# Kernel tuning notes

Measured on AMD Instinct MI355X. Metric: run time of the kernel, lower is better.

The kernel has to match this reference:

```python
import jax, jax.numpy as jnp
import numpy as np

IMAGE_SIZE = 128
FACES_PER_PIXEL = 4
BLUR_RADIUS = 0.01
EPS = 1e-8


def setup_inputs() -> dict:
    key = jax.random.key(0)
    k1, k2, k3 = jax.random.split(key, 3)
    B, V, F = 2, 2000, 800
    # verts are already projected to screen/NDC space: x,y in [-1,1], z > 0 (depth)
    xy = jax.random.uniform(k1, (B, V, 2), minval=-1.0, maxval=1.0)
    z = jax.random.uniform(k2, (B, V, 1), minval=0.5, maxval=2.5)
    verts = jnp.concatenate([xy, z], axis=-1).astype(jnp.float32)
    faces = jax.random.randint(k3, (F, 3), 0, V)
    return {"verts": verts, "faces": faces}


def _edge(a, b, p):
    # signed parallelogram area of (a -> b -> p), using xy components only
    return (p[..., 0] - a[..., 0]) * (b[..., 1] - a[..., 1]) - (
        p[..., 1] - a[..., 1]) * (b[..., 0] - a[..., 0])


def _seg_dist2(p, a, b):
    # squared distance from point p to segment [a, b] in 2D
    ab = b - a
    pa = p - a
    t = jnp.clip(jnp.sum(pa * ab, -1) / (jnp.sum(ab * ab, -1) + EPS), 0.0, 1.0)
    d = pa - t[..., None] * ab
    return jnp.sum(d * d, -1)


def _rasterize(verts, faces):
    H = W = IMAGE_SIZE
    K = FACES_PER_PIXEL
    B = verts.shape[0]
    fv = verts[:, faces]                      # [B,F,3,3] gather face vertices
    v0, v1, v2 = fv[:, :, 0], fv[:, :, 1], fv[:, :, 2]
    a0 = v0[:, None, :, :2]                   # [B,1,F,2]
    a1 = v1[:, None, :, :2]
    a2 = v2[:, None, :, :2]
    z0 = v0[:, None, :, 2]                    # [B,1,F]
    z1 = v1[:, None, :, 2]
    z2 = v2[:, None, :, 2]
    # pixel centers in NDC, pytorch3d convention: index 0 -> +1, last -> -1
    xs = 1.0 - 2.0 * (jnp.arange(W, dtype=verts.dtype) + 0.5) / W
    ys = 1.0 - 2.0 * (jnp.arange(H, dtype=verts.dtype) + 0.5) / H
    yy, xx = jnp.meshgrid(ys, xs, indexing="ij")
    p = jnp.stack([xx, yy], -1).reshape(1, -1, 1, 2)   # [1,P,1,2], P=H*W

    area = _edge(a0, a1, a2)                  # [B,1,F] signed face area*2
    w0 = _edge(a1, a2, p)                     # [B,P,F]
    w1 = _edge(a2, a0, p)
    w2 = _edge(a0, a1, p)
    denom = jnp.where(jnp.abs(area) > EPS, area,
                      jnp.where(area >= 0, EPS, -EPS))
    b0, b1, b2 = w0 / denom, w1 / denom, w2 / denom
    zpix = b0 * z0 + b1 * z1 + b2 * z2        # [B,P,F] interpolated depth

    inside = (b0 >= 0) & (b1 >= 0) & (b2 >= 0)
    dmin = jnp.minimum(_seg_dist2(p, a0, a1),
                       jnp.minimum(_seg_dist2(p, a1, a2),
                                   _seg_dist2(p, a2, a0)))
    dsign = jnp.where(inside, -dmin, dmin)    # signed squared edge distance

    valid = (inside | (dmin < BLUR_RADIUS)) & (zpix > EPS) & (
        jnp.abs(area) > EPS)
    zcand = jnp.where(valid, zpix, jnp.inf)
    _, idx = jax.lax.top_k(-zcand, K)         # K nearest faces per pixel

    take = lambda x: jnp.take_along_axis(x, idx, axis=-1)
    sel_valid = take(valid)
    pix_to_face = jnp.where(sel_valid, idx, -1)
    zbuf = jnp.where(sel_valid, take(zpix), -1.0)
    bary = jnp.stack([b0, b1, b2], -1)        # [B,P,F,3]
    bsel = jnp.take_along_axis(bary, idx[..., None], axis=2)  # [B,P,K,3]
    bsel = jnp.where(sel_valid[..., None], bsel, -1.0)
    dsel = jnp.where(sel_valid, take(dsign), -1.0)

    return (pix_to_face.reshape(B, H, W, K),
            zbuf.reshape(B, H, W, K),
            bsel.reshape(B, H, W, K, 3),
            dsel.reshape(B, H, W, K))


def reference(verts, faces):
    # Fragments: (pix_to_face, zbuf, bary_coords, dists)
    return _rasterize(verts, faces)
```

## Files before the change

### kernel.cpp

```cpp
#include <hip/hip_runtime.h>

#define IMG   128
#define KF    4
#define NF    800
#define NV    2000
#define NB    2
#define EPSF  1e-8f
#define BLURF 0.01f
#define CULL_D2 0.0103f
#define HEXT    0.0547f

typedef unsigned long long u64;
#define INVK ((((u64)0x7f800000u) << 32) | 0xffffffffu)

#pragma clang fp contract(off)

__device__ __forceinline__ float seg_d2(float pax, float pay, float abx, float aby) {
#pragma clang fp contract(off)
    float dd = (abx * abx + aby * aby) + EPSF;
    float t  = (pax * abx + pay * aby) / dd;
    t = fminf(fmaxf(t, 0.0f), 1.0f);
    float dx = pax - t * abx;
    float dy = pay - t * aby;
    return dx * dx + dy * dy;
}

__device__ __forceinline__ void ins4(u64& s0, u64& s1, u64& s2, u64& s3, u64 k) {
    bool c0 = k < s0, c1 = k < s1, c2 = k < s2, c3 = k < s3;
    s3 = c2 ? s2 : (c3 ? k : s3);
    s2 = c1 ? s1 : (c2 ? k : s2);
    s1 = c0 ? s0 : (c1 ? k : s1);
    s0 = c0 ? k  : s0;
}

__global__ __launch_bounds__(256) void raster_p1(
    const float* __restrict__ verts,
    const int*   __restrict__ faces,
    u64* __restrict__ ws,
    int sh)
{
#pragma clang fp contract(off)
    extern __shared__ char dynLDS[];
    __shared__ u64 sK[2 * 4 * 64];
    __shared__ int sTot;

    const int S     = 1 << sh;
    const int chunk = NF >> sh;
    float* sFD  = (float*)dynLDS;
    int*   sList = (int*)(dynLDS + (size_t)chunk * 10 * sizeof(float));

    const int tid   = threadIdx.x;
    const int blk   = blockIdx.x;
    const int tile  = blk >> sh;
    const int slice = blk & (S - 1);
    const int b     = tile >> 8;
    const int trow  = (tile & 255) >> 4;
    const int tcol  = tile & 15;
    const float* vb = verts + b * NV * 3;
    const int fbase = slice * chunk;

    if (tid == 0) sTot = 0;

    for (int j = tid; j < chunk; j += 256) {
        int f = fbase + j;
        int i0 = faces[3 * f + 0], i1 = faces[3 * f + 1], i2 = faces[3 * f + 2];
        float a0x = vb[3 * i0], a0y = vb[3 * i0 + 1], z0 = vb[3 * i0 + 2];
        float a1x = vb[3 * i1], a1y = vb[3 * i1 + 1], z1 = vb[3 * i1 + 2];
        float a2x = vb[3 * i2], a2y = vb[3 * i2 + 1], z2 = vb[3 * i2 + 2];
        float area = (a2x - a0x) * (a1y - a0y) - (a2y - a0y) * (a1x - a0x);
        float aab  = fabsf(area);
        float denom = (aab > EPSF) ? area : (area >= 0.0f ? EPSF : -EPSF);
        float* fd = &sFD[j * 10];
        fd[0] = a0x; fd[1] = a0y; fd[2] = a1x; fd[3] = a1y; fd[4] = a2x; fd[5] = a2y;
        fd[6] = z0;  fd[7] = z1;  fd[8] = z2;  fd[9] = denom;
    }
    __syncthreads();

    const int wave = tid >> 6;
    const int lane = tid & 63;
    const int pr = lane >> 3, pc = lane & 7;
    const int row = trow * 8 + pr, col = tcol * 8 + pc;
    const float px = 1.0f - (2.0f * ((float)col + 0.5f)) / 128.0f;
    const float py = 1.0f - (2.0f * ((float)row + 0.5f)) / 128.0f;
    const float txmax = 1.0f - (2.0f * ((float)(tcol * 8)     + 0.5f)) / 128.0f;
    const float txmin = 1.0f - (2.0f * ((float)(tcol * 8 + 7) + 0.5f)) / 128.0f;
    const float tymax = 1.0f - (2.0f * ((float)(trow * 8)     + 0.5f)) / 128.0f;
    const float tymin = 1.0f - (2.0f * ((float)(trow * 8 + 7) + 0.5f)) / 128.0f;
    const float cx = 0.5f * (txmin + txmax);
    const float cy = 0.5f * (tymin + tymax);

    for (int j = tid; j < chunk; j += 256) {
        const float* fd = &sFD[j * 10];
        float a0x = fd[0], a0y = fd[1], a1x = fd[2], a1y = fd[3], a2x = fd[4], a2y = fd[5];
        float area = (a2x - a0x) * (a1y - a0y) - (a2y - a0y) * (a1x - a0x);
        bool surv = fabsf(area) > EPSF;
        float bxmin = fminf(a0x, fminf(a1x, a2x)) - 0.101f;
        float bxmax = fmaxf(a0x, fmaxf(a1x, a2x)) + 0.101f;
        float bymin = fminf(a0y, fminf(a1y, a2y)) - 0.101f;
        float bymax = fmaxf(a0y, fmaxf(a1y, a2y)) + 0.101f;
        surv &= !(bxmin > txmax || bxmax < txmin || bymin > tymax || bymax < tymin);
        float s = (area >= 0.0f) ? 1.0f : -1.0f;
        float e0x = a2x - a1x, e0y = a2y - a1y;
        float e1x = a0x - a2x, e1y = a0y - a2y;
        float e2x = a1x - a0x, e2y = a1y - a0y;
        float w0 = s * ((cx - a1x) * e0y - (cy - a1y) * e0x) + HEXT * (fabsf(e0x) + fabsf(e0y));
        float w1 = s * ((cx - a2x) * e1y - (cy - a2y) * e1x) + HEXT * (fabsf(e1x) + fabsf(e1y));
        float w2 = s * ((cx - a0x) * e2y - (cy - a0y) * e2x) + HEXT * (fabsf(e2x) + fabsf(e2y));
        float l0 = e0x * e0x + e0y * e0y;
        float l1 = e1x * e1x + e1y * e1y;
        float l2 = e2x * e2x + e2y * e2y;
        surv &= !((w0 < 0.0f) & (w0 * w0 > CULL_D2 * l0));
        surv &= !((w1 < 0.0f) & (w1 * w1 > CULL_D2 * l1));
        surv &= !((w2 < 0.0f) & (w2 * w2 > CULL_D2 * l2));
        if (surv) {
            int pos = atomicAdd(&sTot, 1);
            sList[pos] = j;
        }
    }
    __syncthreads();
    const int total = sTot;

    u64 s0 = INVK, s1 = INVK, s2 = INVK, s3 = INVK;
    for (int j = wave; j < total; j += 4) {
        int lf = sList[j];
        const float* fd = &sFD[lf * 10];
        float a0x = fd[0], a0y = fd[1], a1x = fd[2], a1y = fd[3], a2x = fd[4], a2y = fd[5];
        float z0 = fd[6], z1 = fd[7], z2 = fd[8], denom = fd[9];
        float e0x = a2x - a1x, e0y = a2y - a1y;
        float e1x = a0x - a2x, e1y = a0y - a2y;
        float e2x = a1x - a0x, e2y = a1y - a0y;
        float p0x = px - a0x, p0y = py - a0y;
        float p1x = px - a1x, p1y = py - a1y;
        float p2x = px - a2x, p2y = py - a2y;
        float w0 = p1x * e0y - p1y * e0x;
        float w1 = p2x * e1y - p2y * e1x;
        float w2 = p0x * e2y - p0y * e2x;
        float b0 = w0 / denom, b1 = w1 / denom, b2 = w2 / denom;
        float zpix = (b0 * z0 + b1 * z1) + b2 * z2;
        bool inside = fminf(b0, fminf(b1, b2)) >= 0.0f;
        bool valid;
        if (__all(inside)) {
            valid = (zpix > EPSF);
        } else {
            float dA = seg_d2(p0x, p0y, e2x, e2y);
            float dB = seg_d2(p1x, p1y, e0x, e0y);
            float dC = seg_d2(p2x, p2y, e1x, e1y);
            float dmin = fminf(dA, fminf(dB, dC));
            valid = (inside | (dmin < BLURF)) & (zpix > EPSF);
        }
        u64 key = valid ? ((((u64)__float_as_uint(zpix)) << 32) | (unsigned)(fbase + lf)) : INVK;
        if (__any(key < s3)) ins4(s0, s1, s2, s3, key);
    }

    if (wave >= 2) {
        int r = wave - 2;
        sK[(r * 4 + 0) * 64 + lane] = s0;
        sK[(r * 4 + 1) * 64 + lane] = s1;
        sK[(r * 4 + 2) * 64 + lane] = s2;
        sK[(r * 4 + 3) * 64 + lane] = s3;
    }
    __syncthreads();
    if (wave < 2) {
        ins4(s0, s1, s2, s3, sK[(wave * 4 + 0) * 64 + lane]);
        ins4(s0, s1, s2, s3, sK[(wave * 4 + 1) * 64 + lane]);
        ins4(s0, s1, s2, s3, sK[(wave * 4 + 2) * 64 + lane]);
        ins4(s0, s1, s2, s3, sK[(wave * 4 + 3) * 64 + lane]);
    }
    __syncthreads();
    if (wave == 1) {
        sK[0 * 64 + lane] = s0;
        sK[1 * 64 + lane] = s1;
        sK[2 * 64 + lane] = s2;
        sK[3 * 64 + lane] = s3;
    }
    __syncthreads();
    if (wave == 0) {
        ins4(s0, s1, s2, s3, sK[0 * 64 + lane]);
        ins4(s0, s1, s2, s3, sK[1 * 64 + lane]);
        ins4(s0, s1, s2, s3, sK[2 * 64 + lane]);
        ins4(s0, s1, s2, s3, sK[3 * 64 + lane]);
        u64* wrow = ws + (size_t)blk * 256;
        wrow[0 * 64 + lane] = s0;
        wrow[1 * 64 + lane] = s1;
        wrow[2 * 64 + lane] = s2;
        wrow[3 * 64 + lane] = s3;
    }
}

__global__ __launch_bounds__(256) void raster_p2(
    const float* __restrict__ verts,
    const int*   __restrict__ faces,
    const u64* __restrict__ ws,
    int sh,
    float* __restrict__ out0, float* __restrict__ out1,
    float* __restrict__ out2, float* __restrict__ out3)
{
#pragma clang fp contract(off)
    __shared__ u64 sK[4 * 64];
    const int S    = 1 << sh;
    const int tid  = threadIdx.x;
    const int tile = blockIdx.x;
    const int b    = tile >> 8;
    const int trow = (tile & 255) >> 4;
    const int tcol = tile & 15;
    const float* vb = verts + b * NV * 3;

    if (tid < 64) {
        u64 s0 = INVK, s1 = INVK, s2 = INVK, s3 = INVK;
        const u64* base = ws + (size_t)tile * S * 256;
        for (int s = 0; s < S; ++s) {
            ins4(s0, s1, s2, s3, base[s * 256 + 0 * 64 + tid]);
            ins4(s0, s1, s2, s3, base[s * 256 + 1 * 64 + tid]);
            ins4(s0, s1, s2, s3, base[s * 256 + 2 * 64 + tid]);
            ins4(s0, s1, s2, s3, base[s * 256 + 3 * 64 + tid]);
        }
        sK[0 * 64 + tid] = s0;
        sK[1 * 64 + tid] = s1;
        sK[2 * 64 + tid] = s2;
        sK[3 * 64 + tid] = s3;
    }
    __syncthreads();

    int pix = tid >> 2, k = tid & 3;
    u64 key = sK[k * 64 + pix];
    int prow = pix >> 3, pcol = pix & 7;
    int grow = trow * 8 + prow, gcol = tcol * 8 + pcol;
    int p = (b * IMG + grow) * IMG + gcol;
    float qx = 1.0f - (2.0f * ((float)gcol + 0.5f)) / 128.0f;
    float qy = 1.0f - (2.0f * ((float)grow + 0.5f)) / 128.0f;
    float o0 = -1.0f, o1 = -1.0f, ob0 = -1.0f, ob1 = -1.0f, ob2 = -1.0f, o3 = -1.0f;
    if ((unsigned)(key >> 32) != 0x7f800000u) {
        int fi = (int)(unsigned)(key & 0xffffffffu);
        int i0 = faces[3 * fi + 0], i1 = faces[3 * fi + 1], i2 = faces[3 * fi + 2];
        float a0x = vb[3 * i0], a0y = vb[3 * i0 + 1], z0 = vb[3 * i0 + 2];
        float a1x = vb[3 * i1], a1y = vb[3 * i1 + 1], z1 = vb[3 * i1 + 2];
        float a2x = vb[3 * i2], a2y = vb[3 * i2 + 1], z2 = vb[3 * i2 + 2];
        float area = (a2x - a0x) * (a1y - a0y) - (a2y - a0y) * (a1x - a0x);
        float aab  = fabsf(area);
        float denom = (aab > EPSF) ? area : (area >= 0.0f ? EPSF : -EPSF);
        float e0x = a2x - a1x, e0y = a2y - a1y;
        float e1x = a0x - a2x, e1y = a0y - a2y;
        float e2x = a1x - a0x, e2y = a1y - a0y;
        float p0x = qx - a0x, p0y = qy - a0y;
        float p1x = qx - a1x, p1y = qy - a1y;
        float p2x = qx - a2x, p2y = qy - a2y;
        float w0 = p1x * e0y - p1y * e0x;
        float w1 = p2x * e1y - p2y * e1x;
        float w2 = p0x * e2y - p0y * e2x;
        float b0 = w0 / denom, b1 = w1 / denom, b2 = w2 / denom;
        float zpix = (b0 * z0 + b1 * z1) + b2 * z2;
        bool inside = (b0 >= 0.0f) & (b1 >= 0.0f) & (b2 >= 0.0f);
        float dA = seg_d2(p0x, p0y, e2x, e2y);
        float dB = seg_d2(p1x, p1y, e0x, e0y);
        float dC = seg_d2(p2x, p2y, e1x, e1y);
        float dmin = fminf(dA, fminf(dB, dC));
        o0 = (float)fi;
        o1 = zpix;
        ob0 = b0; ob1 = b1; ob2 = b2;
        o3 = inside ? -dmin : dmin;
    }
    int o = p * KF + k;
    out0[o] = o0;
    out1[o] = o1;
    out2[o * 3 + 0] = ob0;
    out2[o * 3 + 1] = ob1;
    out2[o * 3 + 2] = ob2;
    out3[o] = o3;
}

extern "C" void kernel_launch(void* const* d_in, const int* in_sizes, int n_in,
                              void* d_out, int out_size, void* d_ws, size_t ws_size,
                              hipStream_t stream) {
    const float* verts = (const float*)d_in[0];
    const int*   faces = (const int*)d_in[1];
    float* out = (float*)d_out;
    const int n0 = NB * IMG * IMG * KF;

    const size_t per_slice = 512ull * 256 * sizeof(u64);
    int sh;
    if      (ws_size >= 4 * per_slice) sh = 2;
    else if (ws_size >= 2 * per_slice) sh = 1;
    else                               sh = 0;
    const int S = 1 << sh;
    const int chunk = NF >> sh;
    const size_t dyn = (size_t)chunk * 10 * sizeof(float) + (size_t)chunk * sizeof(int);

    raster_p1<<<dim3(512 * S), dim3(256), dyn, stream>>>(verts, faces, (u64*)d_ws, sh);
    raster_p2<<<dim3(512), dim3(256), 0, stream>>>(verts, faces, (const u64*)d_ws, sh,
        out,
        out + n0,
        out + 2 * n0,
        out + 5 * n0);
}
```

Before: 96.07 us.

## Fuse face setup with culling, compact survivors into LDS, use fast reciprocal division

Merges the face-loading loop into the culling loop, so only surviving faces are written to LDS, as a compact 12-float record read with vector loads. The indirection list goes away. The per-pixel loop replaces IEEE divisions with a refined hardware reciprocal plus a residual correction, and skips the edge-distance work when no lane could enter the top-4. It also allows an 8-way face split when the workspace is large enough, giving more blocks. The denom field now stores the raw area rather than the EPS-clamped value, which is safe only because culled faces have |area|>EPS. The Newton-refined reciprocal may differ from IEEE division in the last bit, and the extra split increases merge work in the second pass.

```diff
diff --git a/kernel.cpp b/kernel.cpp
--- a/kernel.cpp
+++ b/kernel.cpp
@@ -15,6 +15,20 @@
 
 #pragma clang fp contract(off)
 
+__device__ __forceinline__ float rcp2(float d) {
+    float y = __builtin_amdgcn_rcpf(d);
+    float e = __builtin_fmaf(-d, y, 1.0f);
+    y = __builtin_fmaf(y, e, y);
+    e = __builtin_fmaf(-d, y, 1.0f);
+    y = __builtin_fmaf(y, e, y);
+    return y;
+}
+__device__ __forceinline__ float fdivr(float n, float d, float y) {
+    float q0 = n * y;
+    float r  = __builtin_fmaf(-d, q0, n);
+    return __builtin_fmaf(r, y, q0);
+}
+
 __device__ __forceinline__ float seg_d2(float pax, float pay, float abx, float aby) {
 #pragma clang fp contract(off)
     float dd = (abx * abx + aby * aby) + EPSF;
@@ -25,6 +39,18 @@
     return dx * dx + dy * dy;
 }
 
+__device__ __forceinline__ float seg_d2f(float pax, float pay, float abx, float aby) {
+#pragma clang fp contract(off)
+    float dd = (abx * abx + aby * aby) + EPSF;
+    float n  = pax * abx + pay * aby;
+    float y  = rcp2(dd);
+    float t  = fdivr(n, dd, y);
+    t = fminf(fmaxf(t, 0.0f), 1.0f);
+    float dx = pax - t * abx;
+    float dy = pay - t * aby;
+    return dx * dx + dy * dy;
+}
+
 __device__ __forceinline__ void ins4(u64& s0, u64& s1, u64& s2, u64& s3, u64 k) {
     bool c0 = k < s0, c1 = k < s1, c2 = k < s2, c3 = k < s3;
     s3 = c2 ? s2 : (c3 ? k : s3);
@@ -40,14 +66,12 @@
     int sh)
 {
 #pragma clang fp contract(off)
-    extern __shared__ char dynLDS[];
+    extern __shared__ float sFD[];
     __shared__ u64 sK[2 * 4 * 64];
     __shared__ int sTot;
 
     const int S     = 1 << sh;
     const int chunk = NF >> sh;
-    float* sFD  = (float*)dynLDS;
-    int*   sList = (int*)(dynLDS + (size_t)chunk * 10 * sizeof(float));
 
     const int tid   = threadIdx.x;
     const int blk   = blockIdx.x;
@@ -61,37 +85,21 @@
 
     if (tid == 0) sTot = 0;
 
+    const float txmax = 1.0f - (2.0f * ((float)(tcol * 8)     + 0.5f)) / 128.0f;
+    const float txmin = 1.0f - (2.0f * ((float)(tcol * 8 + 7) + 0.5f)) / 128.0f;
+    const float tymax = 1.0f - (2.0f * ((float)(trow * 8)     + 0.5f)) / 128.0f;
+    const float tymin = 1.0f - (2.0f * ((float)(trow * 8 + 7) + 0.5f)) / 128.0f;
+    const float cx = 0.5f * (txmin + txmax);
+    const float cy = 0.5f * (tymin + tymax);
+
+    __syncthreads();
+
     for (int j = tid; j < chunk; j += 256) {
         int f = fbase + j;
         int i0 = faces[3 * f + 0], i1 = faces[3 * f + 1], i2 = faces[3 * f + 2];
         float a0x = vb[3 * i0], a0y = vb[3 * i0 + 1], z0 = vb[3 * i0 + 2];
         float a1x = vb[3 * i1], a1y = vb[3 * i1 + 1], z1 = vb[3 * i1 + 2];
         float a2x = vb[3 * i2], a2y = vb[3 * i2 + 1], z2 = vb[3 * i2 + 2];
-        float area = (a2x - a0x) * (a1y - a0y) - (a2y - a0y) * (a1x - a0x);
-        float aab  = fabsf(area);
-        float denom = (aab > EPSF) ? area : (area >= 0.0f ? EPSF : -EPSF);
-        float* fd = &sFD[j * 10];
-        fd[0] = a0x; fd[1] = a0y; fd[2] = a1x; fd[3] = a1y; fd[4] = a2x; fd[5] = a2y;
-        fd[6] = z0;  fd[7] = z1;  fd[8] = z2;  fd[9] = denom;
-    }
-    __syncthreads();
-
-    const int wave = tid >> 6;
-    const int lane = tid & 63;
-    const int pr = lane >> 3, pc = lane & 7;
-    const int row = trow * 8 + pr, col = tcol * 8 + pc;
-    const float px = 1.0f - (2.0f * ((float)col + 0.5f)) / 128.0f;
-    const float py = 1.0f - (2.0f * ((float)row + 0.5f)) / 128.0f;
-    const float txmax = 1.0f - (2.0f * ((float)(tcol * 8)     + 0.5f)) / 128.0f;
-    const float txmin = 1.0f - (2.0f * ((float)(tcol * 8 + 7) + 0.5f)) / 128.0f;
-    const float tymax = 1.0f - (2.0f * ((float)(trow * 8)     + 0.5f)) / 128.0f;
-    const float tymin = 1.0f - (2.0f * ((float)(trow * 8 + 7) + 0.5f)) / 128.0f;
-    const float cx = 0.5f * (txmin + txmax);
-    const float cy = 0.5f * (tymin + tymax);
-
-    for (int j = tid; j < chunk; j += 256) {
-        const float* fd = &sFD[j * 10];
-        float a0x = fd[0], a0y = fd[1], a1x = fd[2], a1y = fd[3], a2x = fd[4], a2y = fd[5];
         float area = (a2x - a0x) * (a1y - a0y) - (a2y - a0y) * (a1x - a0x);
         bool surv = fabsf(area) > EPSF;
         float bxmin = fminf(a0x, fminf(a1x, a2x)) - 0.101f;
@@ -114,18 +122,33 @@
         surv &= !((w2 < 0.0f) & (w2 * w2 > CULL_D2 * l2));
         if (surv) {
             int pos = atomicAdd(&sTot, 1);
-            sList[pos] = j;
+            float* fd = &sFD[pos * 12];
+            ((float4*)fd)[0] = make_float4(a0x, a0y, a1x, a1y);
+            ((float4*)fd)[1] = make_float4(a2x, a2y, z0, z1);
+            ((float4*)fd)[2] = make_float4(z2, area, __int_as_float(f), 0.0f);
         }
     }
     __syncthreads();
     const int total = sTot;
+
+    const int wave = tid >> 6;
+    const int lane = tid & 63;
+    const int pr = lane >> 3, pc = lane & 7;
+    const int row = trow * 8 + pr, col = tcol * 8 + pc;
+    const float px = 1.0f - (2.0f * ((float)col + 0.5f)) / 128.0f;
+    const float py = 1.0f - (2.0f * ((float)row + 0.5f)) / 128.0f;
 
     u64 s0 = INVK, s1 = INVK, s2 = INVK, s3 = INVK;
     for (int j = wave; j < total; j += 4) {
-        int lf = sList[j];
-        const float* fd = &sFD[lf * 10];
-        float a0x = fd[0], a0y = fd[1], a1x = fd[2], a1y = fd[3], a2x = fd[4], a2y = fd[5];
-        float z0 = fd[6], z1 = fd[7], z2 = fd[8], denom = fd[9];
+        const float* fd = &sFD[j * 12];
+        float4 r0 = ((const float4*)fd)[0];
+        float4 r1 = ((const float4*)fd)[1];
+        float4 r2 = ((const float4*)fd)[2];
+        float a0x = r0.x, a0y = r0.y, a1x = r0.z, a1y = r0.w;
+        float a2x = r1.x, a2y = r1.y, z0 = r1.z, z1 = r1.w;
+        float z2 = r2.x, denom = r2.y;
+        unsigned fi = __float_as_uint(r2.z);
+
         float e0x = a2x - a1x, e0y = a2y - a1y;
         float e1x = a0x - a2x, e1y = a0y - a2y;
         float e2x = a1x - a0x, e2y = a1y - a0y;
@@ -135,21 +158,26 @@
         float w0 = p1x * e0y - p1y * e0x;
         float w1 = p2x * e1y - p2y * e1x;
         float w2 = p0x * e2y - p0y * e2x;
-        float b0 = w0 / denom, b1 = w1 / denom, b2 = w2 / denom;
+        float y  = rcp2(denom);
+        float b0 = fdivr(w0, denom, y);
+        float b1 = fdivr(w1, denom, y);
+        float b2 = fdivr(w2, denom, y);
         float zpix = (b0 * z0 + b1 * z1) + b2 * z2;
         bool inside = fminf(b0, fminf(b1, b2)) >= 0.0f;
-        bool valid;
+
+        u64 okey = (zpix > EPSF) ? ((((u64)__float_as_uint(zpix)) << 32) | (u64)fi) : INVK;
+        if (!__any(okey < s3)) continue;
+
         if (__all(inside)) {
-            valid = (zpix > EPSF);
+            ins4(s0, s1, s2, s3, okey);
         } else {
-            float dA = seg_d2(p0x, p0y, e2x, e2y);
-            float dB = seg_d2(p1x, p1y, e0x, e0y);
-            float dC = seg_d2(p2x, p2y, e1x, e1y);
+            float dA = seg_d2f(p0x, p0y, e2x, e2y);
+            float dB = seg_d2f(p1x, p1y, e0x, e0y);
+            float dC = seg_d2f(p2x, p2y, e1x, e1y);
             float dmin = fminf(dA, fminf(dB, dC));
-            valid = (inside | (dmin < BLURF)) & (zpix > EPSF);
+            u64 key = (inside | (dmin < BLURF)) ? okey : INVK;
+            ins4(s0, s1, s2, s3, key);
         }
-        u64 key = valid ? ((((u64)__float_as_uint(zpix)) << 32) | (unsigned)(fbase + lf)) : INVK;
-        if (__any(key < s3)) ins4(s0, s1, s2, s3, key);
     }
 
     if (wave >= 2) {
@@ -278,14 +306,14 @@
 
     const size_t per_slice = 512ull * 256 * sizeof(u64);
     int sh;
-    if      (ws_size >= 4 * per_slice) sh = 2;
+    if      (ws_size >= 8 * per_slice) sh = 3;
+    else if (ws_size >= 4 * per_slice) sh = 2;
     else if (ws_size >= 2 * per_slice) sh = 1;
     else                               sh = 0;
-    const int S = 1 << sh;
     const int chunk = NF >> sh;
-    const size_t dyn = (size_t)chunk * 10 * sizeof(float) + (size_t)chunk * sizeof(int);
-
-    raster_p1<<<dim3(512 * S), dim3(256), dyn, stream>>>(verts, faces, (u64*)d_ws, sh);
+    const size_t dyn = (size_t)chunk * 12 * sizeof(float);
+
+    raster_p1<<<dim3(512 << sh), dim3(256), dyn, stream>>>(verts, faces, (u64*)d_ws, sh);
     raster_p2<<<dim3(512), dim3(256), 0, stream>>>(verts, faces, (const u64*)d_ws, sh,
         out,
         out + n0,
```

New measurement: 98.17 us. +2.2%, slower.
